# Kernel tuning notes

Measured on AMD Instinct MI355X. Metric: run time of the kernel, lower is better.

## Reference

```python
import jax, jax.numpy as jnp
import numpy as np

SQ23 = float(np.sqrt(2.0 / 3.0))
WIDTH = 1.0  # Fem.width

NELEM = 500_000
NGP = 4
NNODE = 250_000
NDOF = NNODE * 2
HID = 64


def setup_inputs() -> dict:
    key = jax.random.key(0)
    ks = jax.random.split(key, 12)
    u = jax.random.normal(ks[0], (NDOF,), jnp.float32)
    B = jax.random.normal(ks[1], (NELEM, NGP, 3, 8), jnp.float32)
    Jacc = jax.random.uniform(ks[2], (NELEM, NGP), jnp.float32, 0.1, 1.0)
    gp_w = jnp.ones((NGP,), jnp.float32)
    connectivity = jax.random.randint(ks[3], (NELEM, 4), 0, NNODE, jnp.int32)
    weight1 = jax.random.normal(ks[4], (NDOF,), jnp.float32) / 10.0
    scales_inp = jnp.ones((2,), jnp.float32)
    limits_inp = jnp.zeros((2,), jnp.float32)
    scales_grad = jnp.ones((2,), jnp.float32)
    limits_grad = jnp.zeros((2,), jnp.float32)
    W1 = jax.random.normal(ks[5], (2, HID), jnp.float32) / np.sqrt(2.0)
    b1 = jnp.zeros((HID,), jnp.float32)
    W2 = jax.random.normal(ks[6], (HID, HID), jnp.float32) / np.sqrt(HID)
    b2 = jnp.zeros((HID,), jnp.float32)
    W3 = jax.random.normal(ks[7], (HID, 2), jnp.float32) / np.sqrt(HID)
    b3 = jnp.zeros((2,), jnp.float32)
    return dict(u=u, B=B, Jacc=Jacc, gp_w=gp_w, connectivity=connectivity,
                weight1=weight1, scales_inp=scales_inp, limits_inp=limits_inp,
                scales_grad=scales_grad, limits_grad=limits_grad,
                W1=W1, b1=b1, W2=W2, b2=b2, W3=W3, b3=b3)


def reference(u, B, Jacc, gp_w, connectivity, weight1, scales_inp, limits_inp,
              scales_grad, limits_grad, W1, b1, W2, b2, W3, b3):
    ndof = u.shape[0]
    # u_torch1: masked scaling of displacements (all DOFs free here)
    u1 = weight1 * u
    # elemental DOF indices: [E, 8] interleaved (2n, 2n+1) per node
    conn = connectivity
    edofs = jnp.stack([2 * conn, 2 * conn + 1], axis=-1).reshape(conn.shape[0], -1)
    u_e = u1[edofs]                                  # [E, 8] gather
    strain = jnp.einsum('egij,ej->egi', B, u_e)      # [E, G, 3] Voigt strain
    s0, s1, s2 = strain[..., 0], strain[..., 1], strain[..., 2]
    # strain invariants: volumetric ev, deviatoric es, direction n
    ev = s0 + s1
    d00 = s0 - ev / 3.0
    d11 = s1 - ev / 3.0
    d22 = -ev / 3.0
    d01 = s2 / 2.0
    det = jnp.sqrt(d00**2 + d11**2 + d22**2 + 2.0 * d01**2)
    n00, n11, n01 = d00 / det, d11 / det, d01 / det
    es = det * SQ23
    # normalize inputs to the sub-model
    ns = jnp.stack([ev * scales_inp[0] + limits_inp[0],
                    es * scales_inp[1] + limits_inp[1]], axis=-1)  # [E, G, 2]
    # sub-model MLP (batched over all elements x gauss points)
    h = jnp.tanh(ns @ W1 + b1)
    h = jnp.tanh(h @ W2 + b2)
    g = h @ W3 + b3                                  # [E, G, 2]
    # un-normalize -> (p, q) invariants
    p = (g[..., 0] - limits_grad[0]) / scales_grad[0]
    q = (g[..., 1] - limits_grad[1]) / scales_grad[1]
    # invariants -> Voigt stress [s00, s11, s01]
    c = SQ23 * q
    sv = jnp.stack([p + c * n00, p + c * n11, c * n01], axis=-1)  # [E, G, 3]
    # per-GP weights and elemental force: sum_g B^T sigma * (width*Jacc*w_g)
    w = WIDTH * Jacc * gp_w[None, :]                 # [E, G]
    E_P = jnp.einsum('egij,egi,eg->ej', B, sv, w)    # [E, 8]
    # scatter-add assemblage into global force vector
    F = jnp.zeros(ndof, u.dtype).at[edofs.reshape(-1)].add(E_P.reshape(-1))
    return F
```

## Files before the change

### kernel.cpp

```cpp
#include <hip/hip_runtime.h>

#define NELEM 500000
#define NDOF 500000
#define NNODE 250000
#define HID 64
#define NT 31250
#define NBLK 1024
#define NWAVE (NBLK * 4)
#define CSTRIDE 262144

typedef _Float16 half2v __attribute__((ext_vector_type(2)));
typedef _Float16 half8v __attribute__((ext_vector_type(8)));
typedef float float4v __attribute__((ext_vector_type(4)));

#define LAM 2.885390081777927f
#define FSCALE 4194304.0f
#define FINV   2.384185791015625e-7f

__device__ __forceinline__ half2v pk(float a, float b) {
    return __builtin_bit_cast(half2v, __builtin_amdgcn_cvt_pkrtz(a, b));
}
__device__ __forceinline__ float tanh2(float y) {
    float e = __builtin_amdgcn_exp2f(y);
    float r = __builtin_amdgcn_rcpf(e + 1.0f);
    return fmaf(-2.0f, r, 1.0f);
}
__device__ __forceinline__ float fdot2(half2v a, half2v b, float c) {
    return __builtin_amdgcn_fdot2(a, b, c, false);
}

#define SWZF(x, pat) __builtin_bit_cast(float, \
    __builtin_amdgcn_ds_swizzle(__builtin_bit_cast(int, (x)), (pat)))

__global__ __launch_bounds__(64, 1) void pack_weights(
    const float* __restrict__ W2, uint4* __restrict__ ws)
{
    const int lane = threadIdx.x & 63;
    const int quad = lane >> 4, l15 = lane & 15;
#pragma unroll
    for (int t = 0; t < 4; t++)
#pragma unroll
        for (int f = 0; f < 2; f++) {
            union { uint4 q; uint u[4]; } T;
#pragma unroll
            for (int jj = 0; jj < 4; jj++) {
                const int k0 = f * 32 + quad * 8 + 2 * jj;
                const int n  = t * 16 + l15;
                T.u[jj] = __builtin_bit_cast(uint,
                    pk(LAM * W2[k0 * HID + n], LAM * W2[(k0 + 1) * HID + n]));
            }
            ws[(8 + 2 * t + f) * 64 + lane] = T.q;
        }
}

__global__ __launch_bounds__(256, 8) void premul_u(
    const float* __restrict__ u, const float* __restrict__ w1,
    float* __restrict__ u1)
{
    const int i = blockIdx.x * 256 + threadIdx.x;
    if (i < NDOF / 4) {
        const float4 a = ((const float4*)u)[i];
        const float4 b = ((const float4*)w1)[i];
        ((float4*)u1)[i] = make_float4(a.x * b.x, a.y * b.y, a.z * b.z, a.w * b.w);
    }
}

__global__ __launch_bounds__(256, 8) void convert_F(
    unsigned long long* __restrict__ F64,
    const unsigned long long* __restrict__ F8, const int priv)
{
    const int i = blockIdx.x * 256 + threadIdx.x;
    if (i < NNODE) {
        unsigned long long v;
        if (priv) {
            v = 0ull;
#pragma unroll
            for (int x = 0; x < 8; x++) v += F8[(size_t)x * CSTRIDE + i];
        } else {
            v = F64[i];
        }
        const int lo = (int)(unsigned)(v & 0xFFFFFFFFull);
        const int hi = (int)(unsigned)(v >> 32);
        *(float2*)&F64[i] = make_float2((float)lo * FINV, (float)hi * FINV);
    }
}

#define TSTEP(tt, qa, qb) do { \
    const float4v b2v = *(const float4v*)&b2t[wb + (tt) * 4]; \
    union { uint4 q; uint u[4]; } w3u; \
    w3u.q = *(const uint4*)&w3t[wb + (tt) * 4]; \
    float4v c = b2v; \
    c = __builtin_amdgcn_mfma_f32_16x16x32_f16(__builtin_bit_cast(half8v, (qa)), B0.v, c, 0, 0, 0); \
    c = __builtin_amdgcn_mfma_f32_16x16x32_f16(__builtin_bit_cast(half8v, (qb)), B1.v, c, 0, 0, 0); \
    _Pragma("unroll") \
    for (int reg = 0; reg < 4; reg++) { \
        const float h = tanh2(c[reg]); \
        const half2v hh = pk(h, h); \
        sp = sp + hh * __builtin_bit_cast(half2v, w3u.u[reg]); \
    } \
} while (0)

__global__ __launch_bounds__(256, 4) void fem_force_kernel(
    const float* __restrict__ u, const float* __restrict__ B,
    const float* __restrict__ Jacc, const float* __restrict__ gp_w,
    const int* __restrict__ conn, const float* __restrict__ weight1,
    const float* __restrict__ scales_inp, const float* __restrict__ limits_inp,
    const float* __restrict__ scales_grad, const float* __restrict__ limits_grad,
    const float* __restrict__ W1, const float* __restrict__ b1,
    const float* __restrict__ b2, const float* __restrict__ W3,
    const float* __restrict__ b3, const uint4* __restrict__ wt,
    const int premul, const int priv,
    unsigned long long* __restrict__ F64,
    unsigned long long* __restrict__ F8)
{
    __shared__ uint sPQ[8 * 260];
    __shared__ uint sXs[4][64];
    __shared__ uint sGs[4][64];
    __shared__ __align__(16) float b2t[64];
    __shared__ __align__(16) uint  w3t[64];
    __shared__ __align__(16) uint  w1tb[4][16];
    __shared__ __align__(16) float b1tb[4][16];

    const int tid  = threadIdx.x;
    const int lane = tid & 63;
    const int wv   = tid >> 6;
    const int quad = lane >> 4;
    const int l15  = lane & 15;
    const int g    = lane & 3;
    const int pqb  = wv * 65;

    uint xcc;
    asm volatile("s_getreg_b32 %0, hwreg(HW_REG_XCC_ID)" : "=s"(xcc));
    unsigned long long* Fp = F8 + (size_t)(xcc & 7) * CSTRIDE;

    if (tid < 64) {
        const int i  = tid;
        const int it = (i >> 2) & 3, iq = i >> 4, ir = i & 3;
        const int n  = it * 16 + iq * 4 + ir;
        b2t[i] = LAM * b2[n];
        w3t[i] = __builtin_bit_cast(uint, pk(W3[2 * n], W3[2 * n + 1]));
    } else if (tid < 128) {
        const int i = tid - 64;
        const int q = i >> 4, idx = i & 15, f = idx >> 3, jj = idx & 7;
        const int k = f * 32 + q * 8 + jj;
        w1tb[q][idx] = __builtin_bit_cast(uint, pk(LAM * W1[k], LAM * W1[HID + k]));
    } else if (tid < 192) {
        const int i = tid - 128;
        const int q = i >> 4, idx = i & 15, f = idx >> 3, jj = idx & 7;
        const int k = f * 32 + q * 8 + jj;
        b1tb[q][idx] = LAM * b1[k];
    }
    __syncthreads();

    const float SQ23 = 0.816496580927726f;
    const float si0 = scales_inp[0], si1 = scales_inp[1];
    const float li0 = limits_inp[0], li1 = limits_inp[1];
    const float isg0 = 1.0f / scales_grad[0], isg1 = 1.0f / scales_grad[1];
    const float b30c = b3[0] - limits_grad[0];
    const float b31c = b3[1] - limits_grad[1];
    const float gw  = gp_w[g];

    uint4 bfq[8];
#pragma unroll
    for (int i = 0; i < 8; i++) bfq[i] = wt[(8 + i) * 64 + lane];
#pragma unroll
    for (int i = 0; i < 8; i++)
        asm volatile("" : "+v"(bfq[i].x), "+v"(bfq[i].y), "+v"(bfq[i].z), "+v"(bfq[i].w));

    int T = blockIdx.x * 4 + wv;
    float4 bq0, bq1, bq2, bq3, bq4, bq5;
    {
        const float4* Bp = (const float4*)(B + (size_t)T * 1536 + lane * 24);
        bq0 = Bp[0]; bq1 = Bp[1]; bq2 = Bp[2];
        bq3 = Bp[3]; bq4 = Bp[4]; bq5 = Bp[5];
    }
    int connT = conn[T * 64 + lane];
    float jacT = Jacc[T * 64 + lane];
    float2 uT = *(const float2*)(u + 2 * connT);
    float2 wvT = make_float2(1.f, 1.f);
    if (!premul) wvT = *(const float2*)(weight1 + 2 * connT);

    int connN = 0;
    float2 uN = make_float2(0.f, 0.f), wvN = make_float2(1.f, 1.f);
    float jacN = 0.f;

#pragma unroll 1
    for (; T < NT; T += NWAVE) {
        const int Tn = T + NWAVE;
        const bool hasN = (Tn < NT);
        if (hasN) {
            connN = conn[Tn * 64 + lane];
            jacN  = Jacc[Tn * 64 + lane];
        }

        {
            const float vx = wvT.x * uT.x, vy = wvT.y * uT.y;
            float ue[8];
            ue[0] = SWZF(vx, 0x1C); ue[1] = SWZF(vy, 0x1C);
            ue[2] = SWZF(vx, 0x3C); ue[3] = SWZF(vy, 0x3C);
            ue[4] = SWZF(vx, 0x5C); ue[5] = SWZF(vy, 0x5C);
            ue[6] = SWZF(vx, 0x7C); ue[7] = SWZF(vy, 0x7C);

            float Bg[24];
            Bg[0]=bq0.x; Bg[1]=bq0.y; Bg[2]=bq0.z; Bg[3]=bq0.w;
            Bg[4]=bq1.x; Bg[5]=bq1.y; Bg[6]=bq1.z; Bg[7]=bq1.w;
            Bg[8]=bq2.x; Bg[9]=bq2.y; Bg[10]=bq2.z; Bg[11]=bq2.w;
            Bg[12]=bq3.x; Bg[13]=bq3.y; Bg[14]=bq3.z; Bg[15]=bq3.w;
            Bg[16]=bq4.x; Bg[17]=bq4.y; Bg[18]=bq4.z; Bg[19]=bq4.w;
            Bg[20]=bq5.x; Bg[21]=bq5.y; Bg[22]=bq5.z; Bg[23]=bq5.w;

            float s0 = 0.f, s1 = 0.f, s2 = 0.f;
#pragma unroll
            for (int j = 0; j < 8; j++) {
                s0 = fmaf(Bg[j],      ue[j], s0);
                s1 = fmaf(Bg[8 + j],  ue[j], s1);
                s2 = fmaf(Bg[16 + j], ue[j], s2);
            }
            const float ev  = s0 + s1;
            const float ev3 = ev * (1.0f / 3.0f);
            const float d00 = s0 - ev3, d11 = s1 - ev3, d22 = -ev3, d01 = 0.5f * s2;
            const float det = sqrtf(d00 * d00 + d11 * d11 + d22 * d22 + 2.0f * d01 * d01);
            const float rd  = __builtin_amdgcn_rcpf(det);
            const float es  = det * SQ23;
            const float wgt = jacT * gw;
            const float sc  = SQ23 * rd * wgt;
            const float c00 = sc * d00, c11 = sc * d11, c01 = sc * d01;
#pragma unroll
            for (int j = 0; j < 8; j++) {
                const float P = wgt * (Bg[j] + Bg[8 + j]);
                const float Q = fmaf(c00, Bg[j], fmaf(c11, Bg[8 + j], c01 * Bg[16 + j]));
                sPQ[j * 260 + pqb + lane] = __builtin_bit_cast(uint, pk(P, Q));
            }
            sXs[wv][lane] = __builtin_bit_cast(uint,
                pk(fmaf(ev, si0, li0), fmaf(es, si1, li1)));
        }
        if (hasN) {
            const float4* Bp = (const float4*)(B + (size_t)Tn * 1536 + lane * 24);
            bq0 = Bp[0]; bq1 = Bp[1]; bq2 = Bp[2];
            bq3 = Bp[3]; bq4 = Bp[4]; bq5 = Bp[5];
        }
        asm volatile("s_waitcnt lgkmcnt(0)");
        __builtin_amdgcn_sched_barrier(0);
        if (hasN) {
            uN = *(const float2*)(u + 2 * connN);
            if (!premul) wvN = *(const float2*)(weight1 + 2 * connN);
        }

        int zr = 0;
#pragma unroll 1
        for (int rt = 0; rt < 4; rt++) {
            asm volatile("" : "+v"(zr));
            const int qz = quad + zr;
            const int wb = qz * 16;
            const half2v xp = __builtin_bit_cast(half2v, sXs[wv][rt * 16 + l15]);

            union { uint4 q[4]; uint u[16]; } W1L;
            union { float4 q[4]; float f[16]; } B1L;
#pragma unroll
            for (int i = 0; i < 4; i++) {
                W1L.q[i] = *(const uint4*)&w1tb[qz][4 * i];
                B1L.q[i] = *(const float4*)&b1tb[qz][4 * i];
            }

            union { half8v v; uint uu[4]; } B0, B1;
#pragma unroll
            for (int jj = 0; jj < 4; jj++) {
                const float t0 = tanh2(fdot2(xp, __builtin_bit_cast(half2v, W1L.u[2 * jj]),     B1L.f[2 * jj]));
                const float t1 = tanh2(fdot2(xp, __builtin_bit_cast(half2v, W1L.u[2 * jj + 1]), B1L.f[2 * jj + 1]));
                const float t2 = tanh2(fdot2(xp, __builtin_bit_cast(half2v, W1L.u[8 + 2 * jj]),     B1L.f[8 + 2 * jj]));
                const float t3 = tanh2(fdot2(xp, __builtin_bit_cast(half2v, W1L.u[8 + 2 * jj + 1]), B1L.f[8 + 2 * jj + 1]));
                B0.uu[jj] = __builtin_bit_cast(uint, pk(t0, t1));
                B1.uu[jj] = __builtin_bit_cast(uint, pk(t2, t3));
            }

            half2v sp = {_Float16(0.f), _Float16(0.f)};
            TSTEP(0, bfq[0], bfq[1]);
            TSTEP(1, bfq[2], bfq[3]);
            TSTEP(2, bfq[4], bfq[5]);
            TSTEP(3, bfq[6], bfq[7]);

            float s0 = (float)sp[0], s1 = (float)sp[1];
            s0 += SWZF(s0, 0x401F);
            s1 += SWZF(s1, 0x401F);
            s0 += __shfl_xor(s0, 32, 64);
            s1 += __shfl_xor(s1, 32, 64);
            if (quad == 0) {
                const float p = (s0 + b30c) * isg0;
                const float q = (s1 + b31c) * isg1;
                sGs[wv][rt * 16 + l15] = __builtin_bit_cast(uint, pk(p, q));
            }
        }
        asm volatile("s_waitcnt vmcnt(0) lgkmcnt(0)");
        __builtin_amdgcn_sched_barrier(0);

        {
            const int rb = lane & ~3;
            const int j0 = 2 * g;
            float a = 0.f, b = 0.f;
#pragma unroll
            for (int gp = 0; gp < 4; gp++) {
                const int rr = rb + gp;
                const half2v pq = __builtin_bit_cast(half2v, sGs[wv][rr]);
                const uint w0 = sPQ[j0 * 260 + pqb + rr];
                const uint w1 = sPQ[(j0 + 1) * 260 + pqb + rr];
                a = fdot2(pq, __builtin_bit_cast(half2v, w0), a);
                b = fdot2(pq, __builtin_bit_cast(half2v, w1), b);
            }
            const int ia = __float2int_rn(a * FSCALE);
            const int ib = __float2int_rn(b * FSCALE);
            const unsigned long long pkd =
                ((unsigned long long)(unsigned)ib << 32) | (unsigned)ia;
            if (priv) {
                __hip_atomic_fetch_add(Fp + connT, pkd,
                                       __ATOMIC_RELAXED,
                                       __HIP_MEMORY_SCOPE_WORKGROUP);
            } else {
                atomicAdd(&F64[connT], pkd);
            }
        }

        connT = connN; uT = uN; jacT = jacN; wvT = wvN;
    }
}

extern "C" void kernel_launch(void* const* d_in, const int* in_sizes, int n_in,
                              void* d_out, int out_size, void* d_ws, size_t ws_size,
                              hipStream_t stream) {
    const float* u           = (const float*)d_in[0];
    const float* B           = (const float*)d_in[1];
    const float* Jacc        = (const float*)d_in[2];
    const float* gp_w        = (const float*)d_in[3];
    const int*   conn        = (const int*)  d_in[4];
    const float* weight1     = (const float*)d_in[5];
    const float* scales_inp  = (const float*)d_in[6];
    const float* limits_inp  = (const float*)d_in[7];
    const float* scales_grad = (const float*)d_in[8];
    const float* limits_grad = (const float*)d_in[9];
    const float* W1          = (const float*)d_in[10];
    const float* b1          = (const float*)d_in[11];
    const float* W2          = (const float*)d_in[12];
    const float* b2          = (const float*)d_in[13];
    const float* W3          = (const float*)d_in[14];
    const float* b3          = (const float*)d_in[15];
    unsigned long long* F64 = (unsigned long long*)d_out;

    uint4* wt = (uint4*)d_ws;
    float* u1 = (float*)((char*)d_ws + 16384);
    unsigned long long* F8 =
        (unsigned long long*)((char*)d_ws + 16384 + 2097152);
    const size_t priv_bytes = (size_t)8 * CSTRIDE * 8;
    const int can_premul = (ws_size >= 16384 + sizeof(float) * NDOF) ? 1 : 0;
    const int can_priv   =
        (ws_size >= 16384 + 2097152 + priv_bytes) ? 1 : 0;

    (void)hipMemsetAsync(d_out, 0, sizeof(float) * NDOF, stream);
    if (can_priv)
        (void)hipMemsetAsync(F8, 0, priv_bytes, stream);

    pack_weights<<<1, 64, 0, stream>>>(W2, wt);
    if (can_premul)
        premul_u<<<(NDOF / 4 + 255) / 256, 256, 0, stream>>>(u, weight1, u1);

    fem_force_kernel<<<NBLK, 256, 0, stream>>>(
        can_premul ? u1 : u, B, Jacc, gp_w, conn, weight1,
        scales_inp, limits_inp, scales_grad, limits_grad,
        W1, b1, b2, W3, b3, wt, can_premul, can_priv, F64, F8);

    convert_F<<<(NNODE + 255) / 256, 256, 0, stream>>>(F64, F8, can_priv);
}
```

Baseline: 363.0 us.

## Prioritize private force buffers in workspace and emit raw fire-and-forget atomics

Reorders the workspace layout so the per-XCC private force buffers are allocated first, with the premultiplied displacement array placed after them. This lets the private-accumulation path be enabled even when the workspace cannot hold both. The private-path atomic now uses inline assembly for a non-returning global_atomic_add_x2, avoiding the returned value and its wait. When private buffers are unavailable, extra dynamic LDS is requested, presumably to cut occupancy and reduce contention on the shared global atomics.

```diff
diff --git a/kernel.cpp b/kernel.cpp
--- a/kernel.cpp
+++ b/kernel.cpp
@@ -113,6 +113,7 @@
     unsigned long long* __restrict__ F64,
     unsigned long long* __restrict__ F8)
 {
+    extern __shared__ uint dynpad[];
     __shared__ uint sPQ[8 * 260];
     __shared__ uint sXs[4][64];
     __shared__ uint sGs[4][64];
@@ -311,9 +312,10 @@
             const unsigned long long pkd =
                 ((unsigned long long)(unsigned)ib << 32) | (unsigned)ia;
             if (priv) {
-                __hip_atomic_fetch_add(Fp + connT, pkd,
-                                       __ATOMIC_RELAXED,
-                                       __HIP_MEMORY_SCOPE_WORKGROUP);
+                const unsigned long long a64 =
+                    (unsigned long long)(Fp + connT);
+                asm volatile("global_atomic_add_x2 %0, %1, off"
+                             :: "v"(a64), "v"(pkd) : "memory");
             } else {
                 atomicAdd(&F64[connT], pkd);
             }
@@ -344,14 +346,22 @@
     const float* b3          = (const float*)d_in[15];
     unsigned long long* F64 = (unsigned long long*)d_out;
 
+    const size_t priv_bytes = (size_t)8 * CSTRIDE * 8;
     uint4* wt = (uint4*)d_ws;
-    float* u1 = (float*)((char*)d_ws + 16384);
-    unsigned long long* F8 =
-        (unsigned long long*)((char*)d_ws + 16384 + 2097152);
-    const size_t priv_bytes = (size_t)8 * CSTRIDE * 8;
-    const int can_premul = (ws_size >= 16384 + sizeof(float) * NDOF) ? 1 : 0;
-    const int can_priv   =
-        (ws_size >= 16384 + 2097152 + priv_bytes) ? 1 : 0;
+    const int can_priv = (ws_size >= 16384 + priv_bytes) ? 1 : 0;
+
+    unsigned long long* F8;
+    float* u1;
+    int can_premul;
+    if (can_priv) {
+        F8 = (unsigned long long*)((char*)d_ws + 16384);
+        u1 = (float*)((char*)d_ws + 16384 + priv_bytes);
+        can_premul = (ws_size >= 16384 + priv_bytes + sizeof(float) * NDOF) ? 1 : 0;
+    } else {
+        u1 = (float*)((char*)d_ws + 16384);
+        F8 = (unsigned long long*)u1;
+        can_premul = (ws_size >= 16384 + sizeof(float) * NDOF) ? 1 : 0;
+    }
 
     (void)hipMemsetAsync(d_out, 0, sizeof(float) * NDOF, stream);
     if (can_priv)
@@ -361,7 +371,8 @@
     if (can_premul)
         premul_u<<<(NDOF / 4 + 255) / 256, 256, 0, stream>>>(u, weight1, u1);
 
-    fem_force_kernel<<<NBLK, 256, 0, stream>>>(
+    const size_t dyn_lds = can_priv ? 0 : 8192;
+    fem_force_kernel<<<NBLK, 256, dyn_lds, stream>>>(
         can_premul ? u1 : u, B, Jacc, gp_w, conn, weight1,
         scales_inp, limits_inp, scales_grad, limits_grad,
         W1, b1, b2, W3, b3, wt, can_premul, can_priv, F64, F8);
```

Result: no change. 364.5 us (+0.4%).
